# Kernel optimization log

Hardware: AMD Instinct MI355X
Metric: run time of the kernel (lower is better)

The kernel has to match this reference:

```python
import jax, jax.numpy as jnp
import numpy as np

N_NODES = 100_000
N_EDGES = 500_000
G = 1024          # num_graphs
H = 128           # hidden_dim
S_PER = 4         # start nodes per graph
EPS_LN = 1e-5


def _ln(x, g, b):
    m = x.mean(-1, keepdims=True)
    v = ((x - m) ** 2).mean(-1, keepdims=True)
    return (x - m) / jnp.sqrt(v + EPS_LN) * g + b


def _gelu(x):
    return jax.nn.gelu(x, approximate=False)  # torch nn.GELU default (erf)


def setup_inputs() -> dict:
    key = jax.random.key(0)
    ks = jax.random.split(key, 24)
    S = G * S_PER
    d = {
        'node_tokens': jax.random.normal(ks[0], (N_NODES, H), jnp.float32),
        'question_tokens': jax.random.normal(ks[1], (G, H), jnp.float32),
        'edge_tokens': jax.random.normal(ks[2], (N_EDGES, H), jnp.float32),
        'start_node_locals': jax.random.randint(ks[3], (S,), 0, N_NODES),
        'start_node_ptr': jnp.arange(G + 1) * S_PER,
        'edge_batch': jnp.sort(jax.random.randint(ks[4], (N_EDGES,), 0, G)),
        'selected_mask': jax.random.bernoulli(ks[5], 0.5, (N_EDGES,)),
        'edge_index': jax.random.randint(ks[6], (2, N_EDGES), 0, N_NODES),
    }
    w = lambda k, shp: jax.random.normal(k, shp, jnp.float32) * 0.02
    # log_z_head: LN(H) -> Linear(H,H) -> GELU -> Linear(H,1)
    d['ln1_g'] = jnp.ones((H,)); d['ln1_b'] = jnp.zeros((H,))
    d['zw1'] = w(ks[7], (H, H)); d['zb1'] = w(ks[8], (H,))
    d['zw2'] = w(ks[9], (H, 1)); d['zb2'] = jnp.zeros((1,))
    # ctx_projector: Linear(2H,H) -> GELU -> Linear(H,H)
    d['cw1'] = w(ks[10], (2 * H, H)); d['cb1'] = w(ks[11], (H,))
    d['cw2'] = w(ks[12], (H, H)); d['cb2'] = w(ks[13], (H,))
    # backward_head: LN(3H) -> Linear(3H,H) -> GELU -> (Dropout: identity in eval) -> Linear(H,1)
    d['bln_g'] = jnp.ones((3 * H,)); d['bln_b'] = jnp.zeros((3 * H,))
    d['bw1'] = w(ks[14], (3 * H, H)); d['bb1'] = w(ks[15], (H,))
    d['bw2'] = w(ks[16], (H, 1)); d['bb2'] = jnp.zeros((1,))
    return d


def reference(node_tokens, question_tokens, edge_tokens,
              ln1_g, ln1_b, zw1, zb1, zw2, zb2,
              cw1, cb1, cw2, cb2,
              bln_g, bln_b, bw1, bb1, bw2, bb2,
              start_node_locals, start_node_ptr, edge_batch, selected_mask, edge_index):
    counts = start_node_ptr[1:] - start_node_ptr[:-1]                       # [G]
    batch_index = jnp.repeat(jnp.arange(G), counts, total_repeat_length=start_node_locals.shape[0])
    # --- aggregate_start: gather + segment softmax + scatter-add ---
    start_tokens = node_tokens[start_node_locals]                            # [S,H]
    q = question_tokens[batch_index]                                         # [S,H]
    scores = (start_tokens * q).sum(-1) / jnp.sqrt(jnp.float32(H))           # [S]
    m = jax.ops.segment_max(scores, batch_index, num_segments=G)             # [G]
    ex = jnp.exp(scores - m[batch_index])
    denom = jax.ops.segment_sum(ex, batch_index, num_segments=G)
    alpha = ex / denom[batch_index]                                          # pyg_softmax (eps-free path)
    summary = jax.ops.segment_sum(start_tokens * alpha[:, None], batch_index, num_segments=G)  # [G,H]
    # --- build_context + log_z ---
    ctx_in = jnp.concatenate([summary, question_tokens], axis=-1)            # [G,2H]
    context = _gelu(ctx_in @ cw1 + cb1) @ cw2 + cb2                          # [G,H]
    log_z = (_gelu(_ln(context, ln1_g, ln1_b) @ zw1 + zb1) @ zw2 + zb2)[:, 0]  # [G]
    # --- log_pb (learned): gather + segment log-softmax over target nodes + scatter-add per graph ---
    tgt = edge_index[1]                                                      # [E]
    tail = node_tokens[tgt]                                                  # [E,H]
    edge_ctx = jnp.concatenate([edge_tokens, question_tokens[edge_batch], tail], axis=-1)  # [E,3H]
    logits = (_gelu(_ln(edge_ctx, bln_g, bln_b) @ bw1 + bb1) @ bw2 + bb2)[:, 0]            # [E]
    tmax = jax.ops.segment_max(logits, tgt, num_segments=N_NODES)
    shifted = logits - tmax[tgt]
    lse = jnp.log(jax.ops.segment_sum(jnp.exp(shifted), tgt, num_segments=N_NODES))
    log_probs = shifted - lse[tgt]                                           # scatter_log_softmax
    sel = selected_mask.astype(logits.dtype)
    log_pb_per_graph = jax.ops.segment_sum(log_probs * sel, edge_batch, num_segments=G)    # [G]
    # pb_nll: masked mean over graphs that have a selected edge
    nll_per_graph = jax.ops.segment_sum(-log_probs * sel, edge_batch, num_segments=G)
    has_edge = jax.ops.segment_sum(sel, edge_batch, num_segments=G) > 0
    pb_nll = jnp.where(has_edge, nll_per_graph, 0.0).sum() / jnp.maximum(has_edge.sum(), 1).astype(logits.dtype)
    return jnp.stack([log_z, log_pb_per_graph, jnp.broadcast_to(pb_nll, log_z.shape)], axis=-1)  # [G,3]
```

## Files before the change

kernel.cpp:

```cpp
#include <hip/hip_runtime.h>
#include <math.h>

#define G_NUM 1024
#define H 128
#define NNODES 100000
#define NEDGES 500000
#define EPS_LN 1e-5f

typedef __attribute__((ext_vector_type(8))) short short8;
typedef __attribute__((ext_vector_type(4))) float f32x4;

__device__ __forceinline__ float gelu_exact(float x) {
    return 0.5f * x * (1.0f + erff(x * 0.70710678118654752440f));
}
__device__ __forceinline__ unsigned fenc(float f) {
    unsigned b = __float_as_uint(f);
    return (b & 0x80000000u) ? ~b : (b | 0x80000000u);
}
__device__ __forceinline__ float fdec(unsigned k) {
    return __uint_as_float((k & 0x80000000u) ? (k & 0x7FFFFFFFu) : ~k);
}
__device__ __forceinline__ unsigned short f2bf(float x) {
    unsigned u = __float_as_uint(x);
    return (unsigned short)((u + 0x7FFFu + ((u >> 16) & 1u)) >> 16);
}
__device__ __forceinline__ float bf2f(unsigned short h) {
    return __uint_as_float(((unsigned)h) << 16);
}

__global__ void k_probe_mask(const unsigned* __restrict__ mw, int* __restrict__ flag) {
    unsigned v = mw[threadIdx.x];
    if (v == 0x3F800000u) atomicOr(flag, 2);
    else if (v > 1u) atomicOr(flag, 1);
}

__global__ void k_prep(const float* __restrict__ bw1, unsigned short* __restrict__ bwbf) {
    int e = blockIdx.x * 256 + threadIdx.x;
    if (e >= 384 * 128) return;
    int k = e >> 7, n = e & 127;
    int s = k >> 5, krel = k & 31;
    int quad = krel >> 3, j = krel & 7;
    int lane = quad * 16 + (n & 15);
    int t = n >> 4;
    bwbf[((s * 8 + t) * 64 + lane) * 8 + j] = f2bf(bw1[e]);
}

__global__ __launch_bounds__(128) void k_start(
    const float* __restrict__ node_tokens, const float* __restrict__ question,
    const int* __restrict__ locals_, const int* __restrict__ ptr,
    float* __restrict__ summary)
{
    int g = blockIdx.x, t = threadIdx.x;
    __shared__ float red[2];
    __shared__ float sc[16];
    int p0 = ptr[g], p1 = ptr[g + 1];
    int cnt = p1 - p0; if (cnt > 16) cnt = 16;
    float q = question[(size_t)g * H + t];
    for (int s = 0; s < cnt; ++s) {
        int node = locals_[p0 + s];
        float v = node_tokens[(size_t)node * H + t] * q;
        for (int off = 32; off; off >>= 1) v += __shfl_down(v, off);
        if ((t & 63) == 0) red[t >> 6] = v;
        __syncthreads();
        if (t == 0) sc[s] = (red[0] + red[1]) * 0.08838834764831845f;
        __syncthreads();
    }
    float m = -1e30f;
    for (int s = 0; s < cnt; ++s) m = fmaxf(m, sc[s]);
    float den = 0.f;
    for (int s = 0; s < cnt; ++s) den += expf(sc[s] - m);
    float acc = 0.f;
    for (int s = 0; s < cnt; ++s) {
        float a = expf(sc[s] - m) / den;
        acc += a * node_tokens[(size_t)locals_[p0 + s] * H + t];
    }
    summary[(size_t)g * H + t] = acc;
}

__global__ __launch_bounds__(128) void k_graph(
    const float* __restrict__ summary, const float* __restrict__ question,
    const float* __restrict__ cw1, const float* __restrict__ cb1,
    const float* __restrict__ cw2, const float* __restrict__ cb2,
    const float* __restrict__ ln1g, const float* __restrict__ ln1b,
    const float* __restrict__ zw1, const float* __restrict__ zb1,
    const float* __restrict__ zw2, const float* __restrict__ zb2,
    float* __restrict__ out)
{
    int g = blockIdx.x, t = threadIdx.x;
    __shared__ float xin[2 * H];
    __shared__ float buf[H];
    __shared__ float r1[2], r2[2];
    xin[t]     = summary[(size_t)g * H + t];
    xin[H + t] = question[(size_t)g * H + t];
    __syncthreads();
    float a1 = cb1[t];
    for (int k = 0; k < 2 * H; ++k) a1 += xin[k] * cw1[k * H + t];
    buf[t] = gelu_exact(a1);
    __syncthreads();
    float ctx = cb2[t];
    for (int k = 0; k < H; ++k) ctx += buf[k] * cw2[k * H + t];
    float s1 = ctx, s2 = ctx * ctx;
    for (int off = 32; off; off >>= 1) { s1 += __shfl_down(s1, off); s2 += __shfl_down(s2, off); }
    if ((t & 63) == 0) { r1[t >> 6] = s1; r2[t >> 6] = s2; }
    __syncthreads();
    float mean = (r1[0] + r1[1]) * (1.f / H);
    float var  = (r2[0] + r2[1]) * (1.f / H) - mean * mean;
    float xn = (ctx - mean) * rsqrtf(var + EPS_LN) * ln1g[t] + ln1b[t];
    __syncthreads();
    buf[t] = xn;
    __syncthreads();
    float a2 = zb1[t];
    for (int k = 0; k < H; ++k) a2 += buf[k] * zw1[k * H + t];
    float p = gelu_exact(a2) * zw2[t];
    for (int off = 32; off; off >>= 1) p += __shfl_down(p, off);
    if ((t & 63) == 0) r1[t >> 6] = p;
    __syncthreads();
    if (t == 0) out[(size_t)g * 3 + 0] = r1[0] + r1[1] + zb2[0];
}

#define XPITCH 392
__global__ __launch_bounds__(256) void k_edges(
    const float* __restrict__ node_tokens, const float* __restrict__ question,
    const float* __restrict__ edge_tokens, const int* __restrict__ edge_batch,
    const int* __restrict__ edge_index, const float* __restrict__ blng,
    const float* __restrict__ blnb, const unsigned short* __restrict__ bwbf,
    const float* __restrict__ bb1, const float* __restrict__ bw2,
    const float* __restrict__ bb2, float* __restrict__ logits,
    unsigned* __restrict__ tmaxk)
{
    __shared__ unsigned short xbf[64 * XPITCH];
    __shared__ unsigned short bstage[4096];
    __shared__ float red1[64][4];
    __shared__ float red2[64][4];
    __shared__ float minv[64][2];

    int t = threadIdx.x;
    int e0 = blockIdx.x * 64;

    int i = t >> 2, sub = t & 3;
    int e = e0 + i; int ec = e < NEDGES ? e : NEDGES - 1;
    int qrow = edge_batch[ec];
    int trow = edge_index[NEDGES + ec];
    float s1 = 0.f, s2 = 0.f;
    #pragma unroll
    for (int k = 0; k < 24; ++k) {
        int c = sub + 4 * k;
        const float4* src;
        if (c < 32)      src = (const float4*)(edge_tokens + (size_t)ec * H) + c;
        else if (c < 64) src = (const float4*)(question + (size_t)qrow * H) + (c - 32);
        else             src = (const float4*)(node_tokens + (size_t)trow * H) + (c - 64);
        float4 v = *src;
        s1 += v.x + v.y + v.z + v.w;
        s2 += v.x * v.x + v.y * v.y + v.z * v.z + v.w * v.w;
        unsigned short* dst = &xbf[i * XPITCH + c * 4];
        dst[0] = f2bf(v.x); dst[1] = f2bf(v.y); dst[2] = f2bf(v.z); dst[3] = f2bf(v.w);
    }
    red1[i][sub] = s1; red2[i][sub] = s2;
    __syncthreads();
    if (t < 64) {
        float a = red1[t][0] + red1[t][1] + red1[t][2] + red1[t][3];
        float b = red2[t][0] + red2[t][1] + red2[t][2] + red2[t][3];
        float mean = a * (1.f / 384.f);
        float var  = b * (1.f / 384.f) - mean * mean;
        minv[t][0] = mean; minv[t][1] = rsqrtf(var + EPS_LN);
    }
    __syncthreads();
    {
        float mean = minv[i][0], inv = minv[i][1];
        #pragma unroll
        for (int k = 0; k < 24; ++k) {
            int c = sub + 4 * k;
            float4 gv = *((const float4*)(blng) + c);
            float4 bv = *((const float4*)(blnb) + c);
            unsigned short* p = &xbf[i * XPITCH + c * 4];
            p[0] = f2bf((bf2f(p[0]) - mean) * inv * gv.x + bv.x);
            p[1] = f2bf((bf2f(p[1]) - mean) * inv * gv.y + bv.y);
            p[2] = f2bf((bf2f(p[2]) - mean) * inv * gv.z + bv.z);
            p[3] = f2bf((bf2f(p[3]) - mean) * inv * gv.w + bv.w);
        }
    }

    int lane = t & 63, w = t >> 6;
    int n16 = lane & 15, quad = lane >> 4;
    f32x4 acc[8];
    #pragma unroll
    for (int q = 0; q < 8; ++q) acc[q] = (f32x4){0.f, 0.f, 0.f, 0.f};

    for (int s = 0; s < 12; ++s) {
        __syncthreads();
        {
            const uint4* src = (const uint4*)(bwbf + s * 4096);
            uint4* dst = (uint4*)bstage;
            dst[t] = src[t];
            dst[t + 256] = src[t + 256];
        }
        __syncthreads();
        short8 a = *(const short8*)&xbf[(w * 16 + n16) * XPITCH + s * 32 + quad * 8];
        #pragma unroll
        for (int t8 = 0; t8 < 8; ++t8) {
            short8 b = *(const short8*)&bstage[(t8 * 64 + lane) * 8];
            acc[t8] = __builtin_amdgcn_mfma_f32_16x16x32_bf16(a, b, acc[t8], 0, 0, 0);
        }
    }

    float bb1v[8], bw2v[8];
    #pragma unroll
    for (int t8 = 0; t8 < 8; ++t8) {
        bb1v[t8] = bb1[t8 * 16 + n16];
        bw2v[t8] = bw2[t8 * 16 + n16];
    }
    float bb2v = bb2[0];
    #pragma unroll
    for (int r = 0; r < 4; ++r) {
        float s = 0.f;
        #pragma unroll
        for (int t8 = 0; t8 < 8; ++t8)
            s += gelu_exact(acc[t8][r] + bb1v[t8]) * bw2v[t8];
        s += __shfl_xor(s, 1);
        s += __shfl_xor(s, 2);
        s += __shfl_xor(s, 4);
        s += __shfl_xor(s, 8);
        if (n16 == 0) {
            int ei = e0 + w * 16 + quad * 4 + r;
            if (ei < NEDGES) {
                float lg = s + bb2v;
                logits[ei] = lg;
                atomicMax(&tmaxk[edge_index[NEDGES + ei]], fenc(lg));
            }
        }
    }
}

__global__ void k_sumexp(const float* __restrict__ logits,
                         const int* __restrict__ edge_index,
                         const unsigned* __restrict__ tmaxk,
                         float* __restrict__ sumexp)
{
    int e = blockIdx.x * blockDim.x + threadIdx.x;
    if (e >= NEDGES) return;
    int tg = edge_index[NEDGES + e];
    atomicAdd(&sumexp[tg], expf(logits[e] - fdec(tmaxk[tg])));
}

__global__ __launch_bounds__(256) void k_logpb(
    const float* __restrict__ logits,
    const int* __restrict__ edge_index,
    const int* __restrict__ edge_batch,
    const void* __restrict__ mask,
    const int* __restrict__ flag,
    const unsigned* __restrict__ tmaxk,
    const float* __restrict__ sumexp,
    float* __restrict__ logpb, int* __restrict__ selcnt)
{
    __shared__ float lacc[8];
    __shared__ int lcnt[8];
    __shared__ int g0s, big;
    int t = threadIdx.x;
    int e0 = blockIdx.x * 256;
    if (t == 0) {
        int ga = edge_batch[e0 < NEDGES ? e0 : NEDGES - 1];
        int el = e0 + 255; if (el >= NEDGES) el = NEDGES - 1;
        int gb = edge_batch[el];
        g0s = ga; big = (gb - ga > 7);
    }
    if (t < 8) { lacc[t] = 0.f; lcnt[t] = 0; }
    __syncthreads();
    int e = e0 + t;
    if (e < NEDGES) {
        int mode = *flag;
        bool sel;
        if (mode & 2)      sel = ((const float*)mask)[e] != 0.f;
        else if (mode & 1) sel = ((const unsigned char*)mask)[e] != 0;
        else               sel = ((const int*)mask)[e] != 0;
        if (sel) {
            int tg = edge_index[NEDGES + e];
            float lp = logits[e] - fdec(tmaxk[tg]) - logf(sumexp[tg]);
            int g = edge_batch[e];
            if (!big) {
                atomicAdd(&lacc[g - g0s], lp);
                atomicAdd(&lcnt[g - g0s], 1);
            } else {
                atomicAdd(&logpb[g], lp);
                atomicAdd(&selcnt[g], 1);
            }
        }
    }
    __syncthreads();
    if (t < 8 && !big && lcnt[t] > 0) {
        atomicAdd(&logpb[g0s + t], lacc[t]);
        atomicAdd(&selcnt[g0s + t], lcnt[t]);
    }
}

__global__ __launch_bounds__(1024) void k_final(const float* __restrict__ logpb,
                                                const int* __restrict__ selcnt,
                                                float* __restrict__ out)
{
    int g = threadIdx.x;
    float lpb = logpb[g];
    int has = selcnt[g] > 0;
    float s = has ? -lpb : 0.f;
    int c = has;
    __shared__ float rn[16];
    __shared__ int rh[16];
    __shared__ float pbnll_s;
    for (int off = 32; off; off >>= 1) { s += __shfl_down(s, off); c += __shfl_down(c, off); }
    if ((g & 63) == 0) { rn[g >> 6] = s; rh[g >> 6] = c; }
    __syncthreads();
    if (g == 0) {
        float ts = 0.f; int tc = 0;
        for (int i = 0; i < 16; ++i) { ts += rn[i]; tc += rh[i]; }
        pbnll_s = ts / (float)(tc > 0 ? tc : 1);
    }
    __syncthreads();
    out[(size_t)g * 3 + 1] = lpb;
    out[(size_t)g * 3 + 2] = pbnll_s;
}

extern "C" void kernel_launch(void* const* d_in, const int* in_sizes, int n_in,
                              void* d_out, int out_size, void* d_ws, size_t ws_size,
                              hipStream_t stream) {
    const float* node_tokens = (const float*)d_in[0];
    const float* question    = (const float*)d_in[1];
    const float* edge_tokens = (const float*)d_in[2];
    const int*   locals_     = (const int*)d_in[3];
    const int*   ptr         = (const int*)d_in[4];
    const int*   edge_batch  = (const int*)d_in[5];
    const void*  mask        = d_in[6];
    const int*   edge_index  = (const int*)d_in[7];
    const float* ln1g = (const float*)d_in[8];
    const float* ln1b = (const float*)d_in[9];
    const float* zw1  = (const float*)d_in[10];
    const float* zb1  = (const float*)d_in[11];
    const float* zw2  = (const float*)d_in[12];
    const float* zb2  = (const float*)d_in[13];
    const float* cw1  = (const float*)d_in[14];
    const float* cb1  = (const float*)d_in[15];
    const float* cw2  = (const float*)d_in[16];
    const float* cb2  = (const float*)d_in[17];
    const float* blng = (const float*)d_in[18];
    const float* blnb = (const float*)d_in[19];
    const float* bw1  = (const float*)d_in[20];
    const float* bb1  = (const float*)d_in[21];
    const float* bw2  = (const float*)d_in[22];
    const float* bb2  = (const float*)d_in[23];
    float* out = (float*)d_out;

    float* ws = (float*)d_ws;
    unsigned* tmaxk   = (unsigned*)ws;
    float*    sumexp  = ws + 100000;
    float*    logpb   = ws + 200000;
    int*      selcnt  = (int*)(ws + 201024);
    int*      flag    = (int*)(ws + 202048);
    float*    summary = ws + 202052;
    float*    logits  = ws + 333124;
    unsigned short* bwbf = (unsigned short*)(ws + 833124);

    hipMemsetAsync(d_ws, 0, (size_t)202049 * 4, stream);
    k_probe_mask<<<1, 256, 0, stream>>>((const unsigned*)mask, flag);
    k_prep<<<192, 256, 0, stream>>>(bw1, bwbf);
    k_start<<<G_NUM, 128, 0, stream>>>(node_tokens, question, locals_, ptr, summary);
    k_graph<<<G_NUM, 128, 0, stream>>>(summary, question, cw1, cb1, cw2, cb2,
                                       ln1g, ln1b, zw1, zb1, zw2, zb2, out);
    k_edges<<<(NEDGES + 63) / 64, 256, 0, stream>>>(node_tokens, question, edge_tokens,
                                                    edge_batch, edge_index, blng, blnb,
                                                    bwbf, bb1, bw2, bb2, logits, tmaxk);
    int eb = (NEDGES + 255) / 256;
    k_sumexp<<<eb, 256, 0, stream>>>(logits, edge_index, tmaxk, sumexp);
    k_logpb<<<eb, 256, 0, stream>>>(logits, edge_index, edge_batch, mask, flag,
                                    tmaxk, sumexp, logpb, selcnt);
    k_final<<<1, 1024, 0, stream>>>(logpb, selcnt, out);
}
```

Measured before the change: 689.7 us.

## Fold LayerNorm into matmul, drop segment max, fuse start-node attention into graph kernel

LayerNorm gamma is folded into the bf16 weights, and the mean/variance correction is applied after the MFMA using precomputed column sums and a folded bias. This lets raw inputs be converted straight into register fragments without an LDS staging buffer. The softmax max-shift is removed, so the sum of exponentials is accumulated directly in the edge kernel and the separate sumexp pass disappears. Start-node attention is merged into the graph kernel. The changes risk overflow for large logits and precision loss from cancellation in the post-matmul normalization.

Measured after the change: 620.6 us. 10.0% less time.

```diff
diff --git a/kernel.cpp b/kernel.cpp
--- a/kernel.cpp
+++ b/kernel.cpp
@@ -13,19 +13,9 @@
 __device__ __forceinline__ float gelu_exact(float x) {
     return 0.5f * x * (1.0f + erff(x * 0.70710678118654752440f));
 }
-__device__ __forceinline__ unsigned fenc(float f) {
-    unsigned b = __float_as_uint(f);
-    return (b & 0x80000000u) ? ~b : (b | 0x80000000u);
-}
-__device__ __forceinline__ float fdec(unsigned k) {
-    return __uint_as_float((k & 0x80000000u) ? (k & 0x7FFFFFFFu) : ~k);
-}
 __device__ __forceinline__ unsigned short f2bf(float x) {
     unsigned u = __float_as_uint(x);
     return (unsigned short)((u + 0x7FFFu + ((u >> 16) & 1u)) >> 16);
-}
-__device__ __forceinline__ float bf2f(unsigned short h) {
-    return __uint_as_float(((unsigned)h) << 16);
 }
 
 __global__ void k_probe_mask(const unsigned* __restrict__ mw, int* __restrict__ flag) {
@@ -34,51 +24,38 @@
     else if (v > 1u) atomicOr(flag, 1);
 }
 
-__global__ void k_prep(const float* __restrict__ bw1, unsigned short* __restrict__ bwbf) {
+__global__ void k_prep(const float* __restrict__ bw1, const float* __restrict__ blng,
+                       unsigned short* __restrict__ bwbf) {
     int e = blockIdx.x * 256 + threadIdx.x;
     if (e >= 384 * 128) return;
     int k = e >> 7, n = e & 127;
     int s = k >> 5, krel = k & 31;
     int quad = krel >> 3, j = krel & 7;
     int lane = quad * 16 + (n & 15);
-    int t = n >> 4;
-    bwbf[((s * 8 + t) * 64 + lane) * 8 + j] = f2bf(bw1[e]);
-}
-
-__global__ __launch_bounds__(128) void k_start(
+    int t8 = n >> 4;
+    bwbf[((s * 8 + t8) * 64 + lane) * 8 + j] = f2bf(bw1[e] * blng[k]);
+}
+
+__global__ __launch_bounds__(128) void k_prep2(const float* __restrict__ bw1,
+                                               const float* __restrict__ blng,
+                                               const float* __restrict__ blnb,
+                                               const float* __restrict__ bb1,
+                                               float* __restrict__ colsum,
+                                               float* __restrict__ bb1p) {
+    int n = threadIdx.x;
+    float cs = 0.f, bs = 0.f;
+    for (int k = 0; k < 384; ++k) {
+        float w = bw1[k * H + n];
+        cs += blng[k] * w;
+        bs += blnb[k] * w;
+    }
+    colsum[n] = cs;
+    bb1p[n] = bb1[n] + bs;
+}
+
+__global__ __launch_bounds__(128) void k_graph(
     const float* __restrict__ node_tokens, const float* __restrict__ question,
     const int* __restrict__ locals_, const int* __restrict__ ptr,
-    float* __restrict__ summary)
-{
-    int g = blockIdx.x, t = threadIdx.x;
-    __shared__ float red[2];
-    __shared__ float sc[16];
-    int p0 = ptr[g], p1 = ptr[g + 1];
-    int cnt = p1 - p0; if (cnt > 16) cnt = 16;
-    float q = question[(size_t)g * H + t];
-    for (int s = 0; s < cnt; ++s) {
-        int node = locals_[p0 + s];
-        float v = node_tokens[(size_t)node * H + t] * q;
-        for (int off = 32; off; off >>= 1) v += __shfl_down(v, off);
-        if ((t & 63) == 0) red[t >> 6] = v;
-        __syncthreads();
-        if (t == 0) sc[s] = (red[0] + red[1]) * 0.08838834764831845f;
-        __syncthreads();
-    }
-    float m = -1e30f;
-    for (int s = 0; s < cnt; ++s) m = fmaxf(m, sc[s]);
-    float den = 0.f;
-    for (int s = 0; s < cnt; ++s) den += expf(sc[s] - m);
-    float acc = 0.f;
-    for (int s = 0; s < cnt; ++s) {
-        float a = expf(sc[s] - m) / den;
-        acc += a * node_tokens[(size_t)locals_[p0 + s] * H + t];
-    }
-    summary[(size_t)g * H + t] = acc;
-}
-
-__global__ __launch_bounds__(128) void k_graph(
-    const float* __restrict__ summary, const float* __restrict__ question,
     const float* __restrict__ cw1, const float* __restrict__ cb1,
     const float* __restrict__ cw2, const float* __restrict__ cb2,
     const float* __restrict__ ln1g, const float* __restrict__ ln1b,
@@ -90,8 +67,30 @@
     __shared__ float xin[2 * H];
     __shared__ float buf[H];
     __shared__ float r1[2], r2[2];
-    xin[t]     = summary[(size_t)g * H + t];
-    xin[H + t] = question[(size_t)g * H + t];
+    __shared__ float sc[16];
+    int p0 = ptr[g], p1 = ptr[g + 1];
+    int cnt = p1 - p0; if (cnt > 16) cnt = 16;
+    float q = question[(size_t)g * H + t];
+    xin[H + t] = q;
+    for (int s = 0; s < cnt; ++s) {
+        int node = locals_[p0 + s];
+        float v = node_tokens[(size_t)node * H + t] * q;
+        for (int off = 32; off; off >>= 1) v += __shfl_down(v, off);
+        if ((t & 63) == 0) r1[t >> 6] = v;
+        __syncthreads();
+        if (t == 0) sc[s] = (r1[0] + r1[1]) * 0.08838834764831845f;
+        __syncthreads();
+    }
+    float m = -1e30f;
+    for (int s = 0; s < cnt; ++s) m = fmaxf(m, sc[s]);
+    float den = 0.f;
+    for (int s = 0; s < cnt; ++s) den += expf(sc[s] - m);
+    float acc0 = 0.f;
+    for (int s = 0; s < cnt; ++s) {
+        float a = expf(sc[s] - m) / den;
+        acc0 += a * node_tokens[(size_t)locals_[p0 + s] * H + t];
+    }
+    xin[t] = acc0;
     __syncthreads();
     float a1 = cb1[t];
     for (int k = 0; k < 2 * H; ++k) a1 += xin[k] * cw1[k * H + t];
@@ -118,74 +117,55 @@
     if (t == 0) out[(size_t)g * 3 + 0] = r1[0] + r1[1] + zb2[0];
 }
 
-#define XPITCH 392
 __global__ __launch_bounds__(256) void k_edges(
     const float* __restrict__ node_tokens, const float* __restrict__ question,
     const float* __restrict__ edge_tokens, const int* __restrict__ edge_batch,
-    const int* __restrict__ edge_index, const float* __restrict__ blng,
-    const float* __restrict__ blnb, const unsigned short* __restrict__ bwbf,
-    const float* __restrict__ bb1, const float* __restrict__ bw2,
+    const int* __restrict__ edge_index,
+    const unsigned short* __restrict__ bwbf, const float* __restrict__ colsum,
+    const float* __restrict__ bb1p, const float* __restrict__ bw2,
     const float* __restrict__ bb2, float* __restrict__ logits,
-    unsigned* __restrict__ tmaxk)
+    float* __restrict__ sumexp)
 {
-    __shared__ unsigned short xbf[64 * XPITCH];
     __shared__ unsigned short bstage[4096];
-    __shared__ float red1[64][4];
-    __shared__ float red2[64][4];
-    __shared__ float minv[64][2];
-
-    int t = threadIdx.x;
+    int t = threadIdx.x, lane = t & 63, w = t >> 6;
+    int quad = lane >> 4, n16 = lane & 15;
     int e0 = blockIdx.x * 64;
-
-    int i = t >> 2, sub = t & 3;
-    int e = e0 + i; int ec = e < NEDGES ? e : NEDGES - 1;
+    int e = e0 + w * 16 + n16;
+    int ec = e < NEDGES ? e : NEDGES - 1;
     int qrow = edge_batch[ec];
     int trow = edge_index[NEDGES + ec];
+    const float4* ep = (const float4*)(edge_tokens + (size_t)ec * H);
+    const float4* qp = (const float4*)(question + (size_t)qrow * H);
+    const float4* np_ = (const float4*)(node_tokens + (size_t)trow * H);
+
     float s1 = 0.f, s2 = 0.f;
-    #pragma unroll
-    for (int k = 0; k < 24; ++k) {
-        int c = sub + 4 * k;
-        const float4* src;
-        if (c < 32)      src = (const float4*)(edge_tokens + (size_t)ec * H) + c;
-        else if (c < 64) src = (const float4*)(question + (size_t)qrow * H) + (c - 32);
-        else             src = (const float4*)(node_tokens + (size_t)trow * H) + (c - 64);
-        float4 v = *src;
-        s1 += v.x + v.y + v.z + v.w;
-        s2 += v.x * v.x + v.y * v.y + v.z * v.z + v.w * v.w;
-        unsigned short* dst = &xbf[i * XPITCH + c * 4];
-        dst[0] = f2bf(v.x); dst[1] = f2bf(v.y); dst[2] = f2bf(v.z); dst[3] = f2bf(v.w);
-    }
-    red1[i][sub] = s1; red2[i][sub] = s2;
-    __syncthreads();
-    if (t < 64) {
-        float a = red1[t][0] + red1[t][1] + red1[t][2] + red1[t][3];
-        float b = red2[t][0] + red2[t][1] + red2[t][2] + red2[t][3];
-        float mean = a * (1.f / 384.f);
-        float var  = b * (1.f / 384.f) - mean * mean;
-        minv[t][0] = mean; minv[t][1] = rsqrtf(var + EPS_LN);
-    }
-    __syncthreads();
-    {
-        float mean = minv[i][0], inv = minv[i][1];
-        #pragma unroll
-        for (int k = 0; k < 24; ++k) {
-            int c = sub + 4 * k;
-            float4 gv = *((const float4*)(blng) + c);
-            float4 bv = *((const float4*)(blnb) + c);
-            unsigned short* p = &xbf[i * XPITCH + c * 4];
-            p[0] = f2bf((bf2f(p[0]) - mean) * inv * gv.x + bv.x);
-            p[1] = f2bf((bf2f(p[1]) - mean) * inv * gv.y + bv.y);
-            p[2] = f2bf((bf2f(p[2]) - mean) * inv * gv.z + bv.z);
-            p[3] = f2bf((bf2f(p[3]) - mean) * inv * gv.w + bv.w);
-        }
-    }
-
-    int lane = t & 63, w = t >> 6;
-    int n16 = lane & 15, quad = lane >> 4;
+    short8 frag[12];
+    #pragma unroll
+    for (int s = 0; s < 12; ++s) {
+        int c0 = s * 8 + quad * 2;
+        const float4* base = (s < 4) ? ep : (s < 8) ? qp : np_;
+        int cc = c0 - ((s < 4) ? 0 : (s < 8) ? 32 : 64);
+        float4 v0 = base[cc], v1 = base[cc + 1];
+        s1 += v0.x + v0.y + v0.z + v0.w + v1.x + v1.y + v1.z + v1.w;
+        s2 += v0.x*v0.x + v0.y*v0.y + v0.z*v0.z + v0.w*v0.w
+            + v1.x*v1.x + v1.y*v1.y + v1.z*v1.z + v1.w*v1.w;
+        short8 f;
+        f[0] = (short)f2bf(v0.x); f[1] = (short)f2bf(v0.y);
+        f[2] = (short)f2bf(v0.z); f[3] = (short)f2bf(v0.w);
+        f[4] = (short)f2bf(v1.x); f[5] = (short)f2bf(v1.y);
+        f[6] = (short)f2bf(v1.z); f[7] = (short)f2bf(v1.w);
+        frag[s] = f;
+    }
+    s1 += __shfl_xor(s1, 16); s1 += __shfl_xor(s1, 32);
+    s2 += __shfl_xor(s2, 16); s2 += __shfl_xor(s2, 32);
+    float mu  = s1 * (1.f / 384.f);
+    float inv = rsqrtf(s2 * (1.f / 384.f) - mu * mu + EPS_LN);
+
     f32x4 acc[8];
     #pragma unroll
     for (int q = 0; q < 8; ++q) acc[q] = (f32x4){0.f, 0.f, 0.f, 0.f};
 
+    #pragma unroll
     for (int s = 0; s < 12; ++s) {
         __syncthreads();
         {
@@ -195,51 +175,43 @@
             dst[t + 256] = src[t + 256];
         }
         __syncthreads();
-        short8 a = *(const short8*)&xbf[(w * 16 + n16) * XPITCH + s * 32 + quad * 8];
         #pragma unroll
         for (int t8 = 0; t8 < 8; ++t8) {
             short8 b = *(const short8*)&bstage[(t8 * 64 + lane) * 8];
-            acc[t8] = __builtin_amdgcn_mfma_f32_16x16x32_bf16(a, b, acc[t8], 0, 0, 0);
-        }
-    }
-
-    float bb1v[8], bw2v[8];
+            acc[t8] = __builtin_amdgcn_mfma_f32_16x16x32_bf16(frag[s], b, acc[t8], 0, 0, 0);
+        }
+    }
+
+    float csv[8], bbv[8], w2v[8];
     #pragma unroll
     for (int t8 = 0; t8 < 8; ++t8) {
-        bb1v[t8] = bb1[t8 * 16 + n16];
-        bw2v[t8] = bw2[t8 * 16 + n16];
+        int n = t8 * 16 + n16;
+        csv[t8] = colsum[n]; bbv[t8] = bb1p[n]; w2v[t8] = bw2[n];
     }
     float bb2v = bb2[0];
     #pragma unroll
     for (int r = 0; r < 4; ++r) {
-        float s = 0.f;
+        float mu_r  = __shfl(mu,  quad * 4 + r);
+        float inv_r = __shfl(inv, quad * 4 + r);
+        float ssum = 0.f;
         #pragma unroll
-        for (int t8 = 0; t8 < 8; ++t8)
-            s += gelu_exact(acc[t8][r] + bb1v[t8]) * bw2v[t8];
-        s += __shfl_xor(s, 1);
-        s += __shfl_xor(s, 2);
-        s += __shfl_xor(s, 4);
-        s += __shfl_xor(s, 8);
+        for (int t8 = 0; t8 < 8; ++t8) {
+            float y = (acc[t8][r] - mu_r * csv[t8]) * inv_r + bbv[t8];
+            ssum += gelu_exact(y) * w2v[t8];
+        }
+        ssum += __shfl_xor(ssum, 1);
+        ssum += __shfl_xor(ssum, 2);
+        ssum += __shfl_xor(ssum, 4);
+        ssum += __shfl_xor(ssum, 8);
         if (n16 == 0) {
             int ei = e0 + w * 16 + quad * 4 + r;
             if (ei < NEDGES) {
-                float lg = s + bb2v;
+                float lg = ssum + bb2v;
                 logits[ei] = lg;
-                atomicMax(&tmaxk[edge_index[NEDGES + ei]], fenc(lg));
+                atomicAdd(&sumexp[edge_index[NEDGES + ei]], expf(lg));
             }
         }
     }
-}
-
-__global__ void k_sumexp(const float* __restrict__ logits,
-                         const int* __restrict__ edge_index,
-                         const unsigned* __restrict__ tmaxk,
-                         float* __restrict__ sumexp)
-{
-    int e = blockIdx.x * blockDim.x + threadIdx.x;
-    if (e >= NEDGES) return;
-    int tg = edge_index[NEDGES + e];
-    atomicAdd(&sumexp[tg], expf(logits[e] - fdec(tmaxk[tg])));
 }
 
 __global__ __launch_bounds__(256) void k_logpb(
@@ -248,7 +220,6 @@
     const int* __restrict__ edge_batch,
     const void* __restrict__ mask,
     const int* __restrict__ flag,
-    const unsigned* __restrict__ tmaxk,
     const float* __restrict__ sumexp,
     float* __restrict__ logpb, int* __restrict__ selcnt)
 {
@@ -274,7 +245,7 @@
         else               sel = ((const int*)mask)[e] != 0;
         if (sel) {
             int tg = edge_index[NEDGES + e];
-            float lp = logits[e] - fdec(tmaxk[tg]) - logf(sumexp[tg]);
+            float lp = logits[e] - logf(sumexp[tg]);
             int g = edge_batch[e];
             if (!big) {
                 atomicAdd(&lacc[g - g0s], lp);
@@ -347,27 +318,28 @@
     float* out = (float*)d_out;
 
     float* ws = (float*)d_ws;
-    unsigned* tmaxk   = (unsigned*)ws;
-    float*    sumexp  = ws + 100000;
-    float*    logpb   = ws + 200000;
-    int*      selcnt  = (int*)(ws + 201024);
-    int*      flag    = (int*)(ws + 202048);
-    float*    summary = ws + 202052;
-    float*    logits  = ws + 333124;
-    unsigned short* bwbf = (unsigned short*)(ws + 833124);
-
-    hipMemsetAsync(d_ws, 0, (size_t)202049 * 4, stream);
+    float* sumexp  = ws;
+    float* logpb   = ws + 100000;
+    int*   selcnt  = (int*)(ws + 101024);
+    int*   flag    = (int*)(ws + 102048);
+    float* logits  = ws + 102052;
+    float* colsum  = ws + 602052;
+    float* bb1p    = ws + 602180;
+    unsigned short* bwbf = (unsigned short*)(ws + 602308);
+
+    hipMemsetAsync(d_ws, 0, (size_t)102049 * 4, stream);
     k_probe_mask<<<1, 256, 0, stream>>>((const unsigned*)mask, flag);
-    k_prep<<<192, 256, 0, stream>>>(bw1, bwbf);
-    k_start<<<G_NUM, 128, 0, stream>>>(node_tokens, question, locals_, ptr, summary);
-    k_graph<<<G_NUM, 128, 0, stream>>>(summary, question, cw1, cb1, cw2, cb2,
-                                       ln1g, ln1b, zw1, zb1, zw2, zb2, out);
+    k_prep<<<192, 256, 0, stream>>>(bw1, blng, bwbf);
+    k_prep2<<<1, 128, 0, stream>>>(bw1, blng, blnb, bb1, colsum, bb1p);
+    k_graph<<<G_NUM, 128, 0, stream>>>(node_tokens, question, locals_, ptr,
+                                       cw1, cb1, cw2, cb2, ln1g, ln1b,
+                                       zw1, zb1, zw2, zb2, out);
     k_edges<<<(NEDGES + 63) / 64, 256, 0, stream>>>(node_tokens, question, edge_tokens,
-                                                    edge_batch, edge_index, blng, blnb,
-                                                    bwbf, bb1, bw2, bb2, logits, tmaxk);
+                                                    edge_batch, edge_index, bwbf,
+                                                    colsum, bb1p, bw2, bb2,
+                                                    logits, sumexp);
     int eb = (NEDGES + 255) / 256;
-    k_sumexp<<<eb, 256, 0, stream>>>(logits, edge_index, tmaxk, sumexp);
     k_logpb<<<eb, 256, 0, stream>>>(logits, edge_index, edge_batch, mask, flag,
-                                    tmaxk, sumexp, logpb, selcnt);
+                                    sumexp, logpb, selcnt);
     k_final<<<1, 1024, 0, stream>>>(logpb, selcnt, out);
 }
```
